# Kernel tuning notes

Measured on AMD Instinct MI355X. Metric: run time of the kernel, lower is better.

## Reference

```python
import jax, jax.numpy as jnp
import numpy as np

B, D, N, C = 8192, 128, 64, 256

def setup_inputs() -> dict:
    key = jax.random.key(0)
    ks = jax.random.split(key, 7)
    s1 = 1.0 / np.sqrt(D)
    s2 = 1.0 / np.sqrt(C)
    return {
        "X": jax.random.normal(ks[0], (B, D, N), dtype=jnp.float32),
        "W1": jax.random.normal(ks[1], (D, C), dtype=jnp.float32) * s1,
        "b1": jax.random.normal(ks[2], (C,), dtype=jnp.float32) * s1,
        "W2": jax.random.normal(ks[3], (C, C), dtype=jnp.float32) * s2,
        "b2": jax.random.normal(ks[4], (C,), dtype=jnp.float32) * s2,
        "W3": jax.random.normal(ks[5], (C, 1), dtype=jnp.float32) * s2,
        "b3": jax.random.normal(ks[6], (1,), dtype=jnp.float32) * s2,
    }

def reference(X, W1, b1, W2, b2, W3, b3):
    # X: (B, D, N); each per-node slice X[:, :, i] goes through the shared MLP.
    # Batched over nodes: one GEMM instead of N tiny launches.
    h = jax.nn.relu(jnp.einsum('bdn,dc->bnc', X, W1) + b1)   # (B, N, C)
    h = jax.nn.relu(jnp.einsum('bnc,ce->bne', h, W2) + b2)   # (B, N, C)
    logits = jnp.einsum('bnc,co->bno', h, W3) + b3           # (B, N, 1)
    logits = logits[..., 0]                                   # (B, N)
    zeros = jnp.zeros((X.shape[0], 1), dtype=logits.dtype)    # add_zero=True
    return jnp.concatenate([zeros, logits], axis=1)           # (B, N+1)
```

## Files before the change

### kernel.cpp

```cpp
#include <hip/hip_runtime.h>
#include <hip/hip_bf16.h>

typedef unsigned short u16;
typedef unsigned int   u32;
typedef __attribute__((ext_vector_type(8))) short bf16x8;
typedef __attribute__((ext_vector_type(4))) float f32x4;

#define NB 8192

__device__ __forceinline__ u32 pack2bf(float a, float b) {
    __hip_bfloat162 h = __float22bfloat162_rn(make_float2(a, b));
    return *reinterpret_cast<u32*>(&h);
}

__device__ __forceinline__ u16 f2bf(float x) {
    u32 u = __float_as_uint(x);
    u32 r = u + 0x7FFFu + ((u >> 16) & 1u);
    return (u16)(r >> 16);
}

__global__ __launch_bounds__(256) void prep_weights(
    const float* __restrict__ W1, const float* __restrict__ W2,
    u16* __restrict__ w1fr, u16* __restrict__ w2fr)
{
    int tid = blockIdx.x * 256 + threadIdx.x;
    if (tid < 32768) {
        const int f = tid >> 9, r = tid & 511, l = r >> 3, j = r & 7;
        const int p = f >> 3, mt = (f >> 2) & 1, ks = f & 3;
        const int c = 32 * p + 16 * mt + (l & 15);
        const int d = 32 * ks + 8 * (l >> 4) + j;
        w1fr[tid] = f2bf(W1[d * 256 + c]);
    } else {
        const int t2 = tid - 32768;
        if (t2 < 65536) {
            const int f = t2 >> 9, r = t2 & 511, l = r >> 3, j = r & 7;
            const int q = f >> 4, et = (f >> 3) & 1, ks = f & 7;
            const int e = 32 * q + 16 * et + (l & 15);
            const int cc = 32 * ks + 8 * (l >> 4) + j;
            w2fr[t2] = f2bf(W2[cc * 256 + e]);
        }
    }
}

__global__ __launch_bounds__(512, 6) void fused_mlp(
    const float* __restrict__ X,
    const float* __restrict__ b1, const float* __restrict__ b2,
    const float* __restrict__ W3, const float* __restrict__ b3,
    const u16* __restrict__ w1fr, const u16* __restrict__ w2fr,
    float* __restrict__ out)
{
    __shared__ __align__(16) u16 xt[64 * 128];
    __shared__ __align__(16) u16 h1s[64 * 256];
    __shared__ float partl[8][64];

    const int tid = threadIdx.x;
    const int wv  = tid >> 6;
    const int l   = tid & 63;
    const int lc  = l & 15;
    const int lk  = l >> 4;
    const int b   = blockIdx.x;
    const float* Xb = X + (size_t)b * 8192;

    const u16* w1b = w1fr + wv * 4096 + l * 8;
    const u16* w2b = w2fr + wv * 8192 + l * 8;

    #pragma unroll
    for (int c2 = 0; c2 < 2; ++c2) {
        const int dc = wv + 8 * c2, d0 = dc << 3;
        float v[8];
        #pragma unroll
        for (int j = 0; j < 8; ++j) v[j] = Xb[(d0 + j) * 64 + l];
        u32 pk[4];
        #pragma unroll
        for (int j = 0; j < 4; ++j) pk[j] = pack2bf(v[2 * j], v[2 * j + 1]);
        *(uint4*)(xt + l * 128 + ((dc ^ lc) << 3)) = make_uint4(pk[0], pk[1], pk[2], pk[3]);
    }

    bf16x8 afrN[2];
    #pragma unroll
    for (int mt = 0; mt < 2; ++mt)
        afrN[mt] = *(const bf16x8*)(w1b + mt * 2048);
    __syncthreads();

    f32x4 acc[2][4];
    #pragma unroll
    for (int mt = 0; mt < 2; ++mt) {
        const float4 bq = *(const float4*)(b1 + 32 * wv + 16 * mt + 4 * lk);
        #pragma unroll
        for (int nt = 0; nt < 4; ++nt)
            acc[mt][nt] = (f32x4){bq.x, bq.y, bq.z, bq.w};
    }

    #pragma unroll
    for (int ks = 0; ks < 4; ++ks) {
        bf16x8 afr[2], bfr[4];
        #pragma unroll
        for (int mt = 0; mt < 2; ++mt) afr[mt] = afrN[mt];
        if (ks < 3) {
            #pragma unroll
            for (int mt = 0; mt < 2; ++mt)
                afrN[mt] = *(const bf16x8*)(w1b + (mt * 4 + ks + 1) * 512);
        }
        #pragma unroll
        for (int nt = 0; nt < 4; ++nt)
            bfr[nt] = *(const bf16x8*)(xt + (16 * nt + lc) * 128 + (((4 * ks + lk) ^ lc) << 3));
        #pragma unroll
        for (int mt = 0; mt < 2; ++mt)
            #pragma unroll
            for (int nt = 0; nt < 4; ++nt)
                acc[mt][nt] = __builtin_amdgcn_mfma_f32_16x16x32_bf16(afr[mt], bfr[nt], acc[mt][nt], 0, 0, 0);
    }

    #pragma unroll
    for (int mt = 0; mt < 2; ++mt) {
        const int c0 = 32 * wv + 16 * mt + 4 * lk;
        #pragma unroll
        for (int nt = 0; nt < 4; ++nt) {
            const int n = 16 * nt + lc;
            float x0 = fmaxf(acc[mt][nt][0], 0.f);
            float x1 = fmaxf(acc[mt][nt][1], 0.f);
            float x2 = fmaxf(acc[mt][nt][2], 0.f);
            float x3 = fmaxf(acc[mt][nt][3], 0.f);
            const int chunk = (c0 >> 3) ^ lc;
            *(uint2*)(h1s + n * 256 + (chunk << 3) + (c0 & 7)) =
                make_uint2(pack2bf(x0, x1), pack2bf(x2, x3));
        }
    }

    bf16x8 bfrN[2];
    #pragma unroll
    for (int et = 0; et < 2; ++et)
        bfrN[et] = *(const bf16x8*)(w2b + et * 4096);
    __syncthreads();

    f32x4 acc2[4][2];
    float w3v[2];
    #pragma unroll
    for (int et = 0; et < 2; ++et) {
        const int e = 32 * wv + 16 * et + lc;
        const float bv = b2[e];
        w3v[et] = W3[e];
        #pragma unroll
        for (int mt = 0; mt < 4; ++mt)
            acc2[mt][et] = (f32x4){bv, bv, bv, bv};
    }

    #pragma unroll
    for (int ks = 0; ks < 8; ++ks) {
        bf16x8 afr[4], bfr[2];
        #pragma unroll
        for (int et = 0; et < 2; ++et) bfr[et] = bfrN[et];
        if (ks < 7) {
            #pragma unroll
            for (int et = 0; et < 2; ++et)
                bfrN[et] = *(const bf16x8*)(w2b + (et * 8 + ks + 1) * 512);
        }
        #pragma unroll
        for (int mt = 0; mt < 4; ++mt)
            afr[mt] = *(const bf16x8*)(h1s + (16 * mt + lc) * 256 + (((4 * ks + lk) ^ lc) << 3));
        #pragma unroll
        for (int mt = 0; mt < 4; ++mt)
            #pragma unroll
            for (int et = 0; et < 2; ++et)
                acc2[mt][et] = __builtin_amdgcn_mfma_f32_16x16x32_bf16(afr[mt], bfr[et], acc2[mt][et], 0, 0, 0);
    }

    #pragma unroll
    for (int mt = 0; mt < 4; ++mt) {
        #pragma unroll
        for (int j = 0; j < 4; ++j) {
            float s = fmaxf(acc2[mt][0][j], 0.f) * w3v[0]
                    + fmaxf(acc2[mt][1][j], 0.f) * w3v[1];
            s += __shfl_xor(s, 1);
            s += __shfl_xor(s, 2);
            s += __shfl_xor(s, 4);
            s += __shfl_xor(s, 8);
            if (lc == 0) partl[wv][16 * mt + 4 * lk + j] = s;
        }
    }
    __syncthreads();

    if (tid < 64) {
        float s = b3[0];
        #pragma unroll
        for (int k = 0; k < 8; ++k) s += partl[k][tid];
        out[(size_t)b * 65 + 1 + tid] = s;
    } else if (tid == 64) {
        out[(size_t)b * 65] = 0.f;
    }
}

extern "C" void kernel_launch(void* const* d_in, const int* in_sizes, int n_in,
                              void* d_out, int out_size, void* d_ws, size_t ws_size,
                              hipStream_t stream) {
    const float* X  = (const float*)d_in[0];
    const float* W1 = (const float*)d_in[1];
    const float* b1 = (const float*)d_in[2];
    const float* W2 = (const float*)d_in[3];
    const float* b2 = (const float*)d_in[4];
    const float* W3 = (const float*)d_in[5];
    const float* b3 = (const float*)d_in[6];
    float* out = (float*)d_out;

    u16* w1fr = (u16*)d_ws;
    u16* w2fr = w1fr + 32768;

    const int B = in_sizes[0] / (128 * 64);

    prep_weights<<<384, 256, 0, stream>>>(W1, W2, w1fr, w2fr);
    fused_mlp<<<B, 512, 0, stream>>>(X, b1, b2, W3, b3, w1fr, w2fr, out);
}
```

Before: 140.7 us.

## Process two batch rows per block to reuse weight fragments

```diff
diff --git a/kernel.cpp b/kernel.cpp
--- a/kernel.cpp
+++ b/kernel.cpp
@@ -42,38 +42,41 @@
     }
 }
 
-__global__ __launch_bounds__(512, 6) void fused_mlp(
+__global__ __launch_bounds__(512, 4) void fused_mlp(
     const float* __restrict__ X,
     const float* __restrict__ b1, const float* __restrict__ b2,
     const float* __restrict__ W3, const float* __restrict__ b3,
     const u16* __restrict__ w1fr, const u16* __restrict__ w2fr,
     float* __restrict__ out)
 {
-    __shared__ __align__(16) u16 xt[64 * 128];
-    __shared__ __align__(16) u16 h1s[64 * 256];
-    __shared__ float partl[8][64];
+    __shared__ __align__(16) u16 arena[2 * 64 * 256];
+    __shared__ float partl[2][8][64];
 
     const int tid = threadIdx.x;
     const int wv  = tid >> 6;
     const int l   = tid & 63;
     const int lc  = l & 15;
     const int lk  = l >> 4;
-    const int b   = blockIdx.x;
-    const float* Xb = X + (size_t)b * 8192;
+    const int b0  = 2 * blockIdx.x;
 
     const u16* w1b = w1fr + wv * 4096 + l * 8;
     const u16* w2b = w2fr + wv * 8192 + l * 8;
 
     #pragma unroll
-    for (int c2 = 0; c2 < 2; ++c2) {
-        const int dc = wv + 8 * c2, d0 = dc << 3;
-        float v[8];
-        #pragma unroll
-        for (int j = 0; j < 8; ++j) v[j] = Xb[(d0 + j) * 64 + l];
-        u32 pk[4];
-        #pragma unroll
-        for (int j = 0; j < 4; ++j) pk[j] = pack2bf(v[2 * j], v[2 * j + 1]);
-        *(uint4*)(xt + l * 128 + ((dc ^ lc) << 3)) = make_uint4(pk[0], pk[1], pk[2], pk[3]);
+    for (int bb = 0; bb < 2; ++bb) {
+        const float* Xb = X + (size_t)(b0 + bb) * 8192;
+        u16* xt = arena + bb * 8192;
+        #pragma unroll
+        for (int c2 = 0; c2 < 2; ++c2) {
+            const int dc = wv + 8 * c2, d0 = dc << 3;
+            float v[8];
+            #pragma unroll
+            for (int j = 0; j < 8; ++j) v[j] = Xb[(d0 + j) * 64 + l];
+            u32 pk[4];
+            #pragma unroll
+            for (int j = 0; j < 4; ++j) pk[j] = pack2bf(v[2 * j], v[2 * j + 1]);
+            *(uint4*)(xt + l * 128 + ((dc ^ lc) << 3)) = make_uint4(pk[0], pk[1], pk[2], pk[3]);
+        }
     }
 
     bf16x8 afrN[2];
@@ -82,18 +85,20 @@
         afrN[mt] = *(const bf16x8*)(w1b + mt * 2048);
     __syncthreads();
 
-    f32x4 acc[2][4];
+    f32x4 acc[2][2][4];
     #pragma unroll
     for (int mt = 0; mt < 2; ++mt) {
         const float4 bq = *(const float4*)(b1 + 32 * wv + 16 * mt + 4 * lk);
         #pragma unroll
-        for (int nt = 0; nt < 4; ++nt)
-            acc[mt][nt] = (f32x4){bq.x, bq.y, bq.z, bq.w};
+        for (int bb = 0; bb < 2; ++bb)
+            #pragma unroll
+            for (int nt = 0; nt < 4; ++nt)
+                acc[bb][mt][nt] = (f32x4){bq.x, bq.y, bq.z, bq.w};
     }
 
     #pragma unroll
     for (int ks = 0; ks < 4; ++ks) {
-        bf16x8 afr[2], bfr[4];
+        bf16x8 afr[2];
         #pragma unroll
         for (int mt = 0; mt < 2; ++mt) afr[mt] = afrN[mt];
         if (ks < 3) {
@@ -102,28 +107,38 @@
                 afrN[mt] = *(const bf16x8*)(w1b + (mt * 4 + ks + 1) * 512);
         }
         #pragma unroll
-        for (int nt = 0; nt < 4; ++nt)
-            bfr[nt] = *(const bf16x8*)(xt + (16 * nt + lc) * 128 + (((4 * ks + lk) ^ lc) << 3));
-        #pragma unroll
-        for (int mt = 0; mt < 2; ++mt)
+        for (int bb = 0; bb < 2; ++bb) {
+            const u16* xt = arena + bb * 8192;
+            bf16x8 bfr[4];
             #pragma unroll
             for (int nt = 0; nt < 4; ++nt)
-                acc[mt][nt] = __builtin_amdgcn_mfma_f32_16x16x32_bf16(afr[mt], bfr[nt], acc[mt][nt], 0, 0, 0);
-    }
-
-    #pragma unroll
-    for (int mt = 0; mt < 2; ++mt) {
-        const int c0 = 32 * wv + 16 * mt + 4 * lk;
-        #pragma unroll
-        for (int nt = 0; nt < 4; ++nt) {
-            const int n = 16 * nt + lc;
-            float x0 = fmaxf(acc[mt][nt][0], 0.f);
-            float x1 = fmaxf(acc[mt][nt][1], 0.f);
-            float x2 = fmaxf(acc[mt][nt][2], 0.f);
-            float x3 = fmaxf(acc[mt][nt][3], 0.f);
-            const int chunk = (c0 >> 3) ^ lc;
-            *(uint2*)(h1s + n * 256 + (chunk << 3) + (c0 & 7)) =
-                make_uint2(pack2bf(x0, x1), pack2bf(x2, x3));
+                bfr[nt] = *(const bf16x8*)(xt + (16 * nt + lc) * 128 + (((4 * ks + lk) ^ lc) << 3));
+            #pragma unroll
+            for (int mt = 0; mt < 2; ++mt)
+                #pragma unroll
+                for (int nt = 0; nt < 4; ++nt)
+                    acc[bb][mt][nt] = __builtin_amdgcn_mfma_f32_16x16x32_bf16(afr[mt], bfr[nt], acc[bb][mt][nt], 0, 0, 0);
+        }
+    }
+    __syncthreads();
+
+    #pragma unroll
+    for (int bb = 0; bb < 2; ++bb) {
+        u16* h1s = arena + bb * 16384;
+        #pragma unroll
+        for (int mt = 0; mt < 2; ++mt) {
+            const int c0 = 32 * wv + 16 * mt + 4 * lk;
+            #pragma unroll
+            for (int nt = 0; nt < 4; ++nt) {
+                const int n = 16 * nt + lc;
+                float x0 = fmaxf(acc[bb][mt][nt][0], 0.f);
+                float x1 = fmaxf(acc[bb][mt][nt][1], 0.f);
+                float x2 = fmaxf(acc[bb][mt][nt][2], 0.f);
+                float x3 = fmaxf(acc[bb][mt][nt][3], 0.f);
+                const int chunk = (c0 >> 3) ^ lc;
+                *(uint2*)(h1s + n * 256 + (chunk << 3) + (c0 & 7)) =
+                    make_uint2(pack2bf(x0, x1), pack2bf(x2, x3));
+            }
         }
     }
 
@@ -133,7 +148,7 @@
         bfrN[et] = *(const bf16x8*)(w2b + et * 4096);
     __syncthreads();
 
-    f32x4 acc2[4][2];
+    f32x4 acc2[2][4][2];
     float w3v[2];
     #pragma unroll
     for (int et = 0; et < 2; ++et) {
@@ -141,52 +156,65 @@
         const float bv = b2[e];
         w3v[et] = W3[e];
         #pragma unroll
-        for (int mt = 0; mt < 4; ++mt)
-            acc2[mt][et] = (f32x4){bv, bv, bv, bv};
+        for (int bb = 0; bb < 2; ++bb)
+            #pragma unroll
+            for (int mt = 0; mt < 4; ++mt)
+                acc2[bb][mt][et] = (f32x4){bv, bv, bv, bv};
     }
 
     #pragma unroll
     for (int ks = 0; ks < 8; ++ks) {
-        bf16x8 afr[4], bfr[2];
-        #pragma unroll
-        for (int et = 0; et < 2; ++et) bfr[et] = bfrN[et];
+        bf16x8 bfrW[2];
+        #pragma unroll
+        for (int et = 0; et < 2; ++et) bfrW[et] = bfrN[et];
         if (ks < 7) {
             #pragma unroll
             for (int et = 0; et < 2; ++et)
                 bfrN[et] = *(const bf16x8*)(w2b + (et * 8 + ks + 1) * 512);
         }
         #pragma unroll
-        for (int mt = 0; mt < 4; ++mt)
-            afr[mt] = *(const bf16x8*)(h1s + (16 * mt + lc) * 256 + (((4 * ks + lk) ^ lc) << 3));
-        #pragma unroll
-        for (int mt = 0; mt < 4; ++mt)
-            #pragma unroll
-            for (int et = 0; et < 2; ++et)
-                acc2[mt][et] = __builtin_amdgcn_mfma_f32_16x16x32_bf16(afr[mt], bfr[et], acc2[mt][et], 0, 0, 0);
-    }
-
-    #pragma unroll
-    for (int mt = 0; mt < 4; ++mt) {
-        #pragma unroll
-        for (int j = 0; j < 4; ++j) {
-            float s = fmaxf(acc2[mt][0][j], 0.f) * w3v[0]
-                    + fmaxf(acc2[mt][1][j], 0.f) * w3v[1];
-            s += __shfl_xor(s, 1);
-            s += __shfl_xor(s, 2);
-            s += __shfl_xor(s, 4);
-            s += __shfl_xor(s, 8);
-            if (lc == 0) partl[wv][16 * mt + 4 * lk + j] = s;
-        }
-    }
-    __syncthreads();
-
-    if (tid < 64) {
+        for (int bb = 0; bb < 2; ++bb) {
+            const u16* h1s = arena + bb * 16384;
+            bf16x8 afr[4];
+            #pragma unroll
+            for (int mt = 0; mt < 4; ++mt)
+                afr[mt] = *(const bf16x8*)(h1s + (16 * mt + lc) * 256 + (((4 * ks + lk) ^ lc) << 3));
+            #pragma unroll
+            for (int mt = 0; mt < 4; ++mt)
+                #pragma unroll
+                for (int et = 0; et < 2; ++et)
+                    acc2[bb][mt][et] = __builtin_amdgcn_mfma_f32_16x16x32_bf16(afr[mt], bfrW[et], acc2[bb][mt][et], 0, 0, 0);
+        }
+    }
+
+    #pragma unroll
+    for (int bb = 0; bb < 2; ++bb) {
+        #pragma unroll
+        for (int mt = 0; mt < 4; ++mt) {
+            #pragma unroll
+            for (int j = 0; j < 4; ++j) {
+                float s = fmaxf(acc2[bb][mt][0][j], 0.f) * w3v[0]
+                        + fmaxf(acc2[bb][mt][1][j], 0.f) * w3v[1];
+                s += __shfl_xor(s, 1);
+                s += __shfl_xor(s, 2);
+                s += __shfl_xor(s, 4);
+                s += __shfl_xor(s, 8);
+                if (lc == 0) partl[bb][wv][16 * mt + 4 * lk + j] = s;
+            }
+        }
+    }
+    __syncthreads();
+
+    if (tid < 128) {
+        const int bb = tid >> 6, n = tid & 63;
         float s = b3[0];
         #pragma unroll
-        for (int k = 0; k < 8; ++k) s += partl[k][tid];
-        out[(size_t)b * 65 + 1 + tid] = s;
-    } else if (tid == 64) {
-        out[(size_t)b * 65] = 0.f;
+        for (int k = 0; k < 8; ++k) s += partl[bb][k][n];
+        out[(size_t)(b0 + bb) * 65 + 1 + n] = s;
+    } else if (tid == 128) {
+        out[(size_t)b0 * 65] = 0.f;
+    } else if (tid == 129) {
+        out[(size_t)(b0 + 1) * 65] = 0.f;
     }
 }
 
@@ -208,5 +236,5 @@
     const int B = in_sizes[0] / (128 * 64);
 
     prep_weights<<<384, 256, 0, stream>>>(W1, W2, w1fr, w2fr);
-    fused_mlp<<<B, 512, 0, stream>>>(X, b1, b2, W3, b3, w1fr, w2fr, out);
-}
+    fused_mlp<<<B / 2, 512, 0, stream>>>(X, b1, b2, W3, b3, w1fr, w2fr, out);
+}
```

New measurement: 138.1 us. About the same (-1.9%).
